# Kernel tuning notes

Measured on AMD Instinct MI355X. Metric: run time of the kernel, lower is better.

The kernel has to match this reference:

```python
import jax, jax.numpy as jnp
import numpy as np

N_NODES = 100000


def gcn_conv(x, edge_index, W, b):
    """PyG GCNConv: add self-loops, symmetric deg^{-1/2} A deg^{-1/2} aggregation.

    x: [N, Fin], edge_index: [2, E] int (row 0 = src, row 1 = dst).
    Transform first (Fin -> Fout), then gather-normalize-scatter at Fout.
    """
    n = x.shape[0]
    loops = jnp.arange(n, dtype=edge_index.dtype)
    src = jnp.concatenate([edge_index[0], loops])
    dst = jnp.concatenate([edge_index[1], loops])
    # in-degree with self-loops (all edge weights = 1)
    deg = jax.ops.segment_sum(jnp.ones_like(dst, dtype=x.dtype), dst, num_segments=n)
    dinv = jax.lax.rsqrt(deg)  # deg >= 1 thanks to self-loops
    norm = dinv[src] * dinv[dst]  # [E+N]
    h = x @ W  # [N, Fout] dense transform before sparse aggregation
    msgs = norm[:, None] * h[src]  # gather + normalize
    out = jax.ops.segment_sum(msgs, dst, num_segments=n)  # scatter-add
    return out + b


def setup_inputs() -> dict:
    key = jax.random.key(0)
    ks = jax.random.split(key, 8)
    N, E, Fin, H, C = N_NODES, 1600000, 256, 64, 11
    x = jax.random.normal(ks[0], (N, Fin), dtype=jnp.float32)
    edge_index = jax.random.randint(ks[1], (2, E), 0, N, dtype=jnp.int64)
    s1 = 1.0 / np.sqrt(Fin)
    s2 = 1.0 / np.sqrt(H)
    W1 = jax.random.uniform(ks[2], (Fin, H), jnp.float32, -s1, s1)
    b1 = jnp.zeros((H,), jnp.float32)
    W2 = jax.random.uniform(ks[3], (H, H), jnp.float32, -s2, s2)
    b2 = jnp.zeros((H,), jnp.float32)
    Wfc = jax.random.uniform(ks[4], (H, C), jnp.float32, -s2, s2)
    bfc = jax.random.uniform(ks[5], (C,), jnp.float32, -s2, s2)
    return {"x": x, "edge_index": edge_index, "W1": W1, "b1": b1,
            "W2": W2, "b2": b2, "Wfc": Wfc, "bfc": bfc}


def reference(x, edge_index, W1, b1, W2, b2, Wfc, bfc):
    h = jax.nn.relu(gcn_conv(x, edge_index, W1, b1))
    h = jax.nn.relu(gcn_conv(h, edge_index, W2, b2))
    return h @ Wfc + bfc  # [N, 11]
```

## Files before the change

kernel.cpp:

```cpp
#include <hip/hip_runtime.h>
#include <hip/hip_fp16.h>

#define NFEAT 64
#define CE 8192
#define EBUF 4608

typedef _Float16 half8 __attribute__((ext_vector_type(8)));
typedef float f32x4 __attribute__((ext_vector_type(4)));

__device__ __forceinline__ void gll16(const float* g, float* l) {
    __builtin_amdgcn_global_load_lds(
        (const __attribute__((address_space(1))) unsigned int*)g,
        (__attribute__((address_space(3))) unsigned int*)l, 16, 0, 0);
}

__device__ __forceinline__ __half2 bch(unsigned int u) {
    return __builtin_bit_cast(__half2, u);
}

__global__ void k_cvtW(const float* __restrict__ W, __half* __restrict__ Wt, int K) {
    int idx = blockIdx.x * 256 + threadIdx.x;
    if (idx >= 64 * K) return;
    int n = idx / K;
    int k = idx % K;
    Wt[idx] = __float2half(W[(size_t)k * NFEAT + n]);
}

template<int K, bool SCALE, bool CNT>
__global__ __launch_bounds__(256) void k_gemm_x(
    const float* __restrict__ A, const __half* __restrict__ Wt,
    const float* __restrict__ dinv, __half* __restrict__ H, int M,
    const int* __restrict__ eiDst, int* __restrict__ hist, int E)
{
    const int BM = 64, BK = 32;
    __shared__ float As[2 * BM * BK];

    int tid = threadIdx.x;
    int gemmIdx;
    if (CNT) {
        int bid = blockIdx.x;
        int nbkt = (M + 255) >> 8;
        if (bid % 9 == 8) {
            int c = bid / 9;
            int base = c * CE;
            if (base >= E) return;
            int* hb = (int*)As;
            for (int i = tid; i < nbkt; i += 256) hb[i] = 0;
            __syncthreads();
            int hi = min(base + CE, E);
            for (int e = base + tid; e < hi; e += 256)
                atomicAdd(&hb[eiDst[e] >> 8], 1);
            __syncthreads();
            for (int i = tid; i < nbkt; i += 256)
                hist[(size_t)c * nbkt + i] = hb[i];
            return;
        }
        gemmIdx = bid - bid / 9;
    } else {
        gemmIdx = blockIdx.x;
    }
    if (gemmIdx * BM >= M) return;

    int w = tid >> 6, lane = tid & 63;
    int q = lane >> 4, n16 = lane & 15;
    int m0 = gemmIdx * BM;

    auto stage = [&](int k0, int buf) {
#pragma unroll
        for (int rep = 0; rep < 2; ++rep) {
            int cb = (w * 2 + rep) * 64;
            int s = cb + lane;
            int m = s >> 3;
            int kk = (s & 7) ^ (m & 7);
            int row = m0 + m; if (row > M - 1) row = M - 1;
            gll16(A + (size_t)row * K + k0 + kk * 4,
                  &As[buf * (BM * BK) + cb * 4]);
        }
    };

    stage(0, 0);

    f32x4 acc[4];
#pragma unroll
    for (int nt = 0; nt < 4; ++nt) acc[nt] = (f32x4)(0.f);

    const __half* wp = Wt + (size_t)n16 * K + q * 8;

    const int T = K / BK;
    for (int kt = 0; kt < T; ++kt) {
        __syncthreads();
        if (kt + 1 < T) stage((kt + 1) * BK, (kt + 1) & 1);
        const float* As_ = &As[(kt & 1) * (BM * BK)];

        int ml = w * 16 + n16;
        int e0 = (2 * q) ^ (ml & 7);
        int e1 = (2 * q + 1) ^ (ml & 7);
        float4 f0 = *(const float4*)&As_[(ml * 8 + e0) * 4];
        float4 f1 = *(const float4*)&As_[(ml * 8 + e1) * 4];
        float fv[8] = {f0.x, f0.y, f0.z, f0.w, f1.x, f1.y, f1.z, f1.w};
        half8 ahi, alo;
#pragma unroll
        for (int j = 0; j < 8; ++j) {
            _Float16 hi = (_Float16)fv[j];
            ahi[j] = hi;
            alo[j] = (_Float16)(fv[j] - (float)hi);
        }
#pragma unroll
        for (int nt = 0; nt < 4; ++nt) {
            uint4 u = *(const uint4*)(wp + (size_t)(nt * 16) * K + kt * BK);
            half8 b = __builtin_bit_cast(half8, u);
            acc[nt] = __builtin_amdgcn_mfma_f32_16x16x32_f16(ahi, b, acc[nt], 0, 0, 0);
            acc[nt] = __builtin_amdgcn_mfma_f32_16x16x32_f16(alo, b, acc[nt], 0, 0, 0);
        }
        __syncthreads();
    }

#pragma unroll
    for (int reg = 0; reg < 4; ++reg) {
        int row = m0 + w * 16 + q * 4 + reg;
        if (row < M) {
            float di = SCALE ? dinv[row] : 1.0f;
#pragma unroll
            for (int nt = 0; nt < 4; ++nt)
                H[(size_t)row * NFEAT + nt * 16 + n16] =
                    __float2half(di * acc[nt][reg]);
        }
    }
}

__global__ __launch_bounds__(256) void k_scanB(int* __restrict__ hist,
                                               int* __restrict__ cntB,
                                               int nchk, int nbkt) {
    __shared__ int hb[256];
    int b = blockIdx.x, tid = threadIdx.x;
    int v = (tid < nchk) ? hist[(size_t)tid * nbkt + b] : 0;
    hb[tid] = v;
    __syncthreads();
    for (int off = 1; off < 256; off <<= 1) {
        int t = (tid >= off) ? hb[tid - off] : 0;
        __syncthreads();
        if (tid >= off) hb[tid] += t;
        __syncthreads();
    }
    if (tid < nchk) hist[(size_t)tid * nbkt + b] = hb[tid] - v;
    if (tid == 255) cntB[b] = hb[255];
}

__global__ __launch_bounds__(256) void k_scanC(const int* __restrict__ cntB,
                                               int* __restrict__ bb, int nbkt) {
    __shared__ int hb[256];
    int tid = threadIdx.x;
    int i0 = 2 * tid, i1 = 2 * tid + 1;
    int a0 = (i0 < nbkt) ? cntB[i0] : 0;
    int a1 = (i1 < nbkt) ? cntB[i1] : 0;
    hb[tid] = a0 + a1;
    __syncthreads();
    for (int off = 1; off < 256; off <<= 1) {
        int t = (tid >= off) ? hb[tid - off] : 0;
        __syncthreads();
        if (tid >= off) hb[tid] += t;
        __syncthreads();
    }
    int excl = hb[tid] - (a0 + a1);
    if (i0 <= nbkt) bb[i0] = excl;
    if (i1 <= nbkt) bb[i1] = excl + a0;
}

__global__ __launch_bounds__(256) void k_scatter(
    const int* __restrict__ ei, const int* __restrict__ hist,
    const int* __restrict__ bb, int2* __restrict__ E2, int E, int nbkt)
{
    __shared__ int ptr[512];
    int c = blockIdx.x, tid = threadIdx.x;
    for (int i = tid; i < nbkt; i += 256)
        ptr[i] = bb[i] + hist[(size_t)c * nbkt + i];
    __syncthreads();
    int base = c * CE, hi = min(base + CE, E);
    for (int e = base + tid; e < hi; e += 256) {
        int s = ei[e];
        int d = ei[(size_t)E + e];
        int p = atomicAdd(&ptr[d >> 8], 1);
        E2[p] = make_int2(s, d);
    }
}

__global__ __launch_bounds__(256) void k_csr(
    const int2* __restrict__ E2, const int* __restrict__ bb,
    int* __restrict__ rowptr, float* __restrict__ dinv, int* __restrict__ col,
    __half* __restrict__ A, int N, int E)
{
    __shared__ int2 ebuf[EBUF];
    __shared__ int cnt[256];
    __shared__ float dl[256];
    int b = blockIdx.x, tid = threadIdx.x;
    int e0 = bb[b], e1 = bb[b + 1], ne = e1 - e0;
    int nL = min(ne, EBUF);

    cnt[tid] = 0;
    __syncthreads();
    for (int i = tid; i < nL; i += 256) {
        int2 e = E2[e0 + i];
        ebuf[i] = e;
        atomicAdd(&cnt[e.y & 255], 1);
    }
    for (int i = nL + tid; i < ne; i += 256) {
        int2 e = E2[e0 + i];
        atomicAdd(&cnt[e.y & 255], 1);
    }
    __syncthreads();
    int c = cnt[tid];
    dl[tid] = rsqrtf((float)(c + 1));
    for (int off = 1; off < 256; off <<= 1) {
        int t = (tid >= off) ? cnt[tid - off] : 0;
        __syncthreads();
        if (tid >= off) cnt[tid] += t;
        __syncthreads();
    }
    int excl = cnt[tid] - c;
    int node = b * 256 + tid;
    if (node < N) {
        rowptr[node] = e0 + excl;
        dinv[node] = dl[tid];
    }
    if (b == 0 && tid == 0) rowptr[N] = E;
    __syncthreads();
    cnt[tid] = excl;
    __syncthreads();
    for (int i = tid; i < nL; i += 256) {
        int2 e = ebuf[i];
        int p = atomicAdd(&cnt[e.y & 255], 1);
        col[e0 + p] = e.x;
    }
    for (int i = nL + tid; i < ne; i += 256) {
        int2 e = E2[e0 + i];
        int p = atomicAdd(&cnt[e.y & 255], 1);
        col[e0 + p] = e.x;
    }

    for (int it = tid; it < 256 * 8; it += 256) {
        int ln = it >> 3;
        int node2 = b * 256 + ln;
        if (node2 < N) {
            float di = dl[ln];
            uint4* p = (uint4*)A + (size_t)node2 * 8 + (it & 7);
            uint4 u = *p;
            auto sc = [&](unsigned int x) {
                float2 f = __half22float2(bch(x));
                return __builtin_bit_cast(unsigned int,
                       __float22half2_rn(make_float2(f.x * di, f.y * di)));
            };
            u.x = sc(u.x); u.y = sc(u.y); u.z = sc(u.z); u.w = sc(u.w);
            *p = u;
        }
    }
}

template<bool FC>
__global__ __launch_bounds__(256) void k_aggr(
    const __half* __restrict__ h, const int* __restrict__ rowptr,
    const int* __restrict__ col, const float* __restrict__ dinv,
    const float* __restrict__ bias, const float* __restrict__ Wfc,
    const float* __restrict__ bfc, float* __restrict__ out, int n)
{
    __shared__ float Wl[NFEAT * 11 + 11];
    int tid = threadIdx.x;
    if (FC) {
        for (int i = tid; i < NFEAT * 11; i += 256) Wl[i] = Wfc[i];
        if (tid < 11) Wl[NFEAT * 11 + tid] = bfc[tid];
        __syncthreads();
    }
    int lane = tid & 63;
    int li = lane & 7;
    int fi = li << 3;
    int r = blockIdx.x * 32 + ((tid >> 6) << 3) + (lane >> 3);
    bool valid = r < n;

    int beg = 0, end = 0;
    if (valid) { beg = rowptr[r]; end = rowptr[r + 1]; }

    const __half* hp = h + fi;
    auto ld = [&](int src) { return *(const uint4*)(hp + (size_t)src * NFEAT); };

    float a0 = 0.f, a1 = 0.f, a2 = 0.f, a3 = 0.f,
          a4 = 0.f, a5 = 0.f, a6 = 0.f, a7 = 0.f;
    auto addu = [&](uint4 u) {
        float2 f0 = __half22float2(bch(u.x));
        float2 f1 = __half22float2(bch(u.y));
        float2 f2 = __half22float2(bch(u.z));
        float2 f3 = __half22float2(bch(u.w));
        a0 += f0.x; a1 += f0.y; a2 += f1.x; a3 += f1.y;
        a4 += f2.x; a5 += f2.y; a6 += f3.x; a7 += f3.y;
    };

    if (valid) addu(ld(r));
    int j = beg;
    for (; j + 1 < end; j += 2) {
        uint4 u0 = ld(col[j]);
        uint4 u1 = ld(col[j + 1]);
        uint4 s;
        s.x = __builtin_bit_cast(unsigned int, __hadd2(bch(u0.x), bch(u1.x)));
        s.y = __builtin_bit_cast(unsigned int, __hadd2(bch(u0.y), bch(u1.y)));
        s.z = __builtin_bit_cast(unsigned int, __hadd2(bch(u0.z), bch(u1.z)));
        s.w = __builtin_bit_cast(unsigned int, __hadd2(bch(u0.w), bch(u1.w)));
        addu(s);
    }
    if (j < end) addu(ld(col[j]));

    if (!valid) return;
    float di = dinv[r];
    float t0 = fmaxf(bias[fi + 0] + di * a0, 0.f);
    float t1 = fmaxf(bias[fi + 1] + di * a1, 0.f);
    float t2 = fmaxf(bias[fi + 2] + di * a2, 0.f);
    float t3 = fmaxf(bias[fi + 3] + di * a3, 0.f);
    float t4 = fmaxf(bias[fi + 4] + di * a4, 0.f);
    float t5 = fmaxf(bias[fi + 5] + di * a5, 0.f);
    float t6 = fmaxf(bias[fi + 6] + di * a6, 0.f);
    float t7 = fmaxf(bias[fi + 7] + di * a7, 0.f);

    if (!FC) {
        float4 lo = make_float4(t0, t1, t2, t3);
        float4 hi = make_float4(t4, t5, t6, t7);
        float* op = out + (size_t)r * NFEAT + fi;
        *(float4*)op = lo;
        *(float4*)(op + 4) = hi;
    } else {
#pragma unroll
        for (int c = 0; c < 11; ++c) {
            const float* wc = &Wl[fi * 11 + c];
            float p = t0 * wc[0] + t1 * wc[11] + t2 * wc[22] + t3 * wc[33]
                    + t4 * wc[44] + t5 * wc[55] + t6 * wc[66] + t7 * wc[77];
            p += __shfl_xor(p, 1, 64);
            p += __shfl_xor(p, 2, 64);
            p += __shfl_xor(p, 4, 64);
            if (li == 0) out[(size_t)r * 11 + c] = p + Wl[NFEAT * 11 + c];
        }
    }
}

extern "C" void kernel_launch(void* const* d_in, const int* in_sizes, int n_in,
                              void* d_out, int out_size, void* d_ws, size_t ws_size,
                              hipStream_t stream) {
    const float* x   = (const float*)d_in[0];
    const int*   ei  = (const int*)d_in[1];
    const float* W1  = (const float*)d_in[2];
    const float* b1  = (const float*)d_in[3];
    const float* W2  = (const float*)d_in[4];
    const float* b2  = (const float*)d_in[5];
    const float* Wfc = (const float*)d_in[6];
    const float* bfc = (const float*)d_in[7];
    float* out = (float*)d_out;

    const int Fin = 256;
    int N = in_sizes[0] / Fin;
    int E = in_sizes[1] / 2;

    char* ws = (char*)d_ws;
    size_t off = 0;
    auto alloc = [&](size_t bytes) { void* p = ws + off; off = (off + bytes + 255) & ~(size_t)255; return p; };
    int*    rowptr = (int*)   alloc((size_t)(N + 1) * 4);
    float*  dinv   = (float*) alloc((size_t)N * 4);
    int*    col    = (int*)   alloc((size_t)E * 4);
    __half* Wt1    = (__half*)alloc((size_t)64 * 256 * 2);
    __half* Wt2    = (__half*)alloc((size_t)64 * 64 * 2);
    __half* A      = (__half*)alloc((size_t)N * NFEAT * 2);
    float*  B      = (float*) alloc((size_t)N * NFEAT * 4);

    int NBKT = (N + 255) >> 8;
    int NCHK = (E + CE - 1) / CE;

    int2* E2   = (int2*)B;
    int*  hist = (int*)B + (size_t)2 * E;
    int*  bb   = hist + (size_t)NCHK * NBKT;
    int*  cntB = bb + NBKT + 1;

    int gE2 = NCHK;
    int gb  = (N + 63) / 64;
    int gA  = (N + 31) / 32;
    int g9  = 9 * max(NCHK, (gb + 7) / 8);

    k_cvtW<<<(64 * 256 + 255) / 256, 256, 0, stream>>>(W1, Wt1, 256);
    k_cvtW<<<(64 * 64 + 255) / 256, 256, 0, stream>>>(W2, Wt2, 64);

    k_gemm_x<256, false, true><<<g9, 256, 0, stream>>>(
        x, Wt1, nullptr, A, N, ei + E, hist, E);

    k_scanB<<<NBKT, 256, 0, stream>>>(hist, cntB, NCHK, NBKT);
    k_scanC<<<1, 256, 0, stream>>>(cntB, bb, NBKT);
    k_scatter<<<gE2, 256, 0, stream>>>(ei, hist, bb, E2, E, NBKT);
    k_csr<<<NBKT, 256, 0, stream>>>(E2, bb, rowptr, dinv, col, A, N, E);

    k_aggr<false><<<gA, 256, 0, stream>>>(A, rowptr, col, dinv, b1, nullptr, nullptr, B, N);

    k_gemm_x<64, true, false><<<gb, 256, 0, stream>>>(
        B, Wt2, dinv, A, N, nullptr, nullptr, 0);
    k_aggr<true><<<gA, 256, 0, stream>>>(A, rowptr, col, dinv, b2, Wfc, bfc, out, N);
}
```

Measured before the change: 327.1 us.

## Fuse layer-1 aggregation with layer-2 GEMM and restructure the preprocessing pipeline

Merges the two weight conversions and the edge histogram into a single prep kernel. The layer-1 GEMM now runs after CSR construction so it can apply the dinv scaling directly, which removes the separate rescale pass over A in k_csr. A new fused kernel aggregates layer 1 into shared memory and runs the 64x64 layer-2 GEMM with split-fp16 MFMA, so the fp32 intermediate no longer makes a global round-trip. The aggregation loops are unrolled to four gathers per iteration. In exchange, the big GEMM no longer overlaps with the histogram, and the fused kernel uses more LDS per block.

```diff
diff --git a/kernel.cpp b/kernel.cpp
--- a/kernel.cpp
+++ b/kernel.cpp
@@ -18,47 +18,46 @@
     return __builtin_bit_cast(__half2, u);
 }
 
-__global__ void k_cvtW(const float* __restrict__ W, __half* __restrict__ Wt, int K) {
-    int idx = blockIdx.x * 256 + threadIdx.x;
-    if (idx >= 64 * K) return;
-    int n = idx / K;
-    int k = idx % K;
-    Wt[idx] = __float2half(W[(size_t)k * NFEAT + n]);
-}
-
-template<int K, bool SCALE, bool CNT>
+__global__ __launch_bounds__(256) void k_prep(
+    const float* __restrict__ W1, __half* __restrict__ Wt1,
+    const float* __restrict__ W2, __half* __restrict__ Wt2,
+    const int* __restrict__ eiDst, int* __restrict__ hist, int E, int nbkt)
+{
+    __shared__ int hb[512];
+    int bid = blockIdx.x, tid = threadIdx.x;
+    if (bid < 64) {
+        int idx = bid * 256 + tid;
+        int n = idx >> 8, k = idx & 255;
+        Wt1[idx] = __float2half(W1[(size_t)k * NFEAT + n]);
+    } else if (bid < 80) {
+        int idx = (bid - 64) * 256 + tid;
+        int n = idx >> 6, k = idx & 63;
+        Wt2[idx] = __float2half(W2[(size_t)k * NFEAT + n]);
+    } else {
+        int c = bid - 80;
+        int base = c * CE;
+        if (base >= E) return;
+        for (int i = tid; i < nbkt; i += 256) hb[i] = 0;
+        __syncthreads();
+        int hi = min(base + CE, E);
+        for (int e = base + tid; e < hi; e += 256)
+            atomicAdd(&hb[eiDst[e] >> 8], 1);
+        __syncthreads();
+        for (int i = tid; i < nbkt; i += 256)
+            hist[(size_t)c * nbkt + i] = hb[i];
+    }
+}
+
+template<int K, bool SCALE>
 __global__ __launch_bounds__(256) void k_gemm_x(
     const float* __restrict__ A, const __half* __restrict__ Wt,
-    const float* __restrict__ dinv, __half* __restrict__ H, int M,
-    const int* __restrict__ eiDst, int* __restrict__ hist, int E)
+    const float* __restrict__ dinv, __half* __restrict__ H, int M)
 {
     const int BM = 64, BK = 32;
     __shared__ float As[2 * BM * BK];
 
     int tid = threadIdx.x;
-    int gemmIdx;
-    if (CNT) {
-        int bid = blockIdx.x;
-        int nbkt = (M + 255) >> 8;
-        if (bid % 9 == 8) {
-            int c = bid / 9;
-            int base = c * CE;
-            if (base >= E) return;
-            int* hb = (int*)As;
-            for (int i = tid; i < nbkt; i += 256) hb[i] = 0;
-            __syncthreads();
-            int hi = min(base + CE, E);
-            for (int e = base + tid; e < hi; e += 256)
-                atomicAdd(&hb[eiDst[e] >> 8], 1);
-            __syncthreads();
-            for (int i = tid; i < nbkt; i += 256)
-                hist[(size_t)c * nbkt + i] = hb[i];
-            return;
-        }
-        gemmIdx = bid - bid / 9;
-    } else {
-        gemmIdx = blockIdx.x;
-    }
+    int gemmIdx = blockIdx.x;
     if (gemmIdx * BM >= M) return;
 
     int w = tid >> 6, lane = tid & 63;
@@ -187,7 +186,7 @@
 __global__ __launch_bounds__(256) void k_csr(
     const int2* __restrict__ E2, const int* __restrict__ bb,
     int* __restrict__ rowptr, float* __restrict__ dinv, int* __restrict__ col,
-    __half* __restrict__ A, int N, int E)
+    int N, int E)
 {
     __shared__ int2 ebuf[EBUF];
     __shared__ int cnt[256];
@@ -236,27 +235,116 @@
         int p = atomicAdd(&cnt[e.y & 255], 1);
         col[e0 + p] = e.x;
     }
-
-    for (int it = tid; it < 256 * 8; it += 256) {
-        int ln = it >> 3;
-        int node2 = b * 256 + ln;
-        if (node2 < N) {
-            float di = dl[ln];
-            uint4* p = (uint4*)A + (size_t)node2 * 8 + (it & 7);
-            uint4 u = *p;
-            auto sc = [&](unsigned int x) {
-                float2 f = __half22float2(bch(x));
-                return __builtin_bit_cast(unsigned int,
-                       __float22half2_rn(make_float2(f.x * di, f.y * di)));
+}
+
+__global__ __launch_bounds__(256) void k_ag1g2(
+    const __half* __restrict__ h, const int* __restrict__ rowptr,
+    const int* __restrict__ col, const float* __restrict__ dinv,
+    const float* __restrict__ b1, const __half* __restrict__ Wt2,
+    __half* __restrict__ H2, int n)
+{
+    __shared__ float Bs[64][68];
+    int tid = threadIdx.x;
+    int w = tid >> 6, lane = tid & 63;
+    int li = lane & 7, fi = li << 3;
+    int slot = (w << 3) | (lane >> 3);
+
+    const __half* hp = h + fi;
+    auto ld = [&](int src) { return *(const uint4*)(hp + (size_t)src * NFEAT); };
+
+#pragma unroll
+    for (int hf = 0; hf < 2; ++hf) {
+        int lr = hf * 32 + slot;
+        int r = blockIdx.x * 64 + lr;
+        float t0 = 0.f, t1 = 0.f, t2 = 0.f, t3 = 0.f,
+              t4 = 0.f, t5 = 0.f, t6 = 0.f, t7 = 0.f;
+        if (r < n) {
+            float a0 = 0.f, a1 = 0.f, a2 = 0.f, a3 = 0.f,
+                  a4 = 0.f, a5 = 0.f, a6 = 0.f, a7 = 0.f;
+            auto addu = [&](uint4 u) {
+                float2 f0 = __half22float2(bch(u.x));
+                float2 f1 = __half22float2(bch(u.y));
+                float2 f2 = __half22float2(bch(u.z));
+                float2 f3 = __half22float2(bch(u.w));
+                a0 += f0.x; a1 += f0.y; a2 += f1.x; a3 += f1.y;
+                a4 += f2.x; a5 += f2.y; a6 += f3.x; a7 += f3.y;
             };
-            u.x = sc(u.x); u.y = sc(u.y); u.z = sc(u.z); u.w = sc(u.w);
-            *p = u;
-        }
-    }
-}
-
-template<bool FC>
-__global__ __launch_bounds__(256) void k_aggr(
+            auto p2 = [&](uint4 u0, uint4 u1) {
+                uint4 s;
+                s.x = __builtin_bit_cast(unsigned int, __hadd2(bch(u0.x), bch(u1.x)));
+                s.y = __builtin_bit_cast(unsigned int, __hadd2(bch(u0.y), bch(u1.y)));
+                s.z = __builtin_bit_cast(unsigned int, __hadd2(bch(u0.z), bch(u1.z)));
+                s.w = __builtin_bit_cast(unsigned int, __hadd2(bch(u0.w), bch(u1.w)));
+                addu(s);
+            };
+            int beg = rowptr[r], end = rowptr[r + 1];
+            addu(ld(r));
+            int j = beg;
+            for (; j + 3 < end; j += 4) {
+                uint4 u0 = ld(col[j]);
+                uint4 u1 = ld(col[j + 1]);
+                uint4 u2 = ld(col[j + 2]);
+                uint4 u3 = ld(col[j + 3]);
+                p2(u0, u1);
+                p2(u2, u3);
+            }
+            for (; j < end; ++j) addu(ld(col[j]));
+            float di = dinv[r];
+            t0 = fmaxf(b1[fi + 0] + di * a0, 0.f);
+            t1 = fmaxf(b1[fi + 1] + di * a1, 0.f);
+            t2 = fmaxf(b1[fi + 2] + di * a2, 0.f);
+            t3 = fmaxf(b1[fi + 3] + di * a3, 0.f);
+            t4 = fmaxf(b1[fi + 4] + di * a4, 0.f);
+            t5 = fmaxf(b1[fi + 5] + di * a5, 0.f);
+            t6 = fmaxf(b1[fi + 6] + di * a6, 0.f);
+            t7 = fmaxf(b1[fi + 7] + di * a7, 0.f);
+        }
+        *(float4*)&Bs[lr][fi]     = make_float4(t0, t1, t2, t3);
+        *(float4*)&Bs[lr][fi + 4] = make_float4(t4, t5, t6, t7);
+    }
+    __syncthreads();
+
+    int q = lane >> 4, n16 = lane & 15;
+    f32x4 acc[4];
+#pragma unroll
+    for (int nt = 0; nt < 4; ++nt) acc[nt] = (f32x4)(0.f);
+    const __half* wp = Wt2 + (size_t)n16 * 64 + q * 8;
+
+#pragma unroll
+    for (int kt = 0; kt < 2; ++kt) {
+        const float* ap = &Bs[w * 16 + n16][kt * 32 + q * 8];
+        float4 f0 = *(const float4*)ap;
+        float4 f1 = *(const float4*)(ap + 4);
+        float fv[8] = {f0.x, f0.y, f0.z, f0.w, f1.x, f1.y, f1.z, f1.w};
+        half8 ahi, alo;
+#pragma unroll
+        for (int j = 0; j < 8; ++j) {
+            _Float16 hi = (_Float16)fv[j];
+            ahi[j] = hi;
+            alo[j] = (_Float16)(fv[j] - (float)hi);
+        }
+#pragma unroll
+        for (int nt = 0; nt < 4; ++nt) {
+            uint4 u = *(const uint4*)(wp + (size_t)(nt * 16) * 64 + kt * 32);
+            half8 b = __builtin_bit_cast(half8, u);
+            acc[nt] = __builtin_amdgcn_mfma_f32_16x16x32_f16(ahi, b, acc[nt], 0, 0, 0);
+            acc[nt] = __builtin_amdgcn_mfma_f32_16x16x32_f16(alo, b, acc[nt], 0, 0, 0);
+        }
+    }
+#pragma unroll
+    for (int reg = 0; reg < 4; ++reg) {
+        int row = blockIdx.x * 64 + w * 16 + q * 4 + reg;
+        if (row < n) {
+            float di = dinv[row];
+#pragma unroll
+            for (int nt = 0; nt < 4; ++nt)
+                H2[(size_t)row * NFEAT + nt * 16 + n16] =
+                    __float2half(di * acc[nt][reg]);
+        }
+    }
+}
+
+__global__ __launch_bounds__(256) void k_aggr2(
     const __half* __restrict__ h, const int* __restrict__ rowptr,
     const int* __restrict__ col, const float* __restrict__ dinv,
     const float* __restrict__ bias, const float* __restrict__ Wfc,
@@ -264,11 +352,10 @@
 {
     __shared__ float Wl[NFEAT * 11 + 11];
     int tid = threadIdx.x;
-    if (FC) {
-        for (int i = tid; i < NFEAT * 11; i += 256) Wl[i] = Wfc[i];
-        if (tid < 11) Wl[NFEAT * 11 + tid] = bfc[tid];
-        __syncthreads();
-    }
+    for (int i = tid; i < NFEAT * 11; i += 256) Wl[i] = Wfc[i];
+    if (tid < 11) Wl[NFEAT * 11 + tid] = bfc[tid];
+    __syncthreads();
+
     int lane = tid & 63;
     int li = lane & 7;
     int fi = li << 3;
@@ -291,20 +378,26 @@
         a0 += f0.x; a1 += f0.y; a2 += f1.x; a3 += f1.y;
         a4 += f2.x; a5 += f2.y; a6 += f3.x; a7 += f3.y;
     };
-
-    if (valid) addu(ld(r));
-    int j = beg;
-    for (; j + 1 < end; j += 2) {
-        uint4 u0 = ld(col[j]);
-        uint4 u1 = ld(col[j + 1]);
+    auto p2 = [&](uint4 u0, uint4 u1) {
         uint4 s;
         s.x = __builtin_bit_cast(unsigned int, __hadd2(bch(u0.x), bch(u1.x)));
         s.y = __builtin_bit_cast(unsigned int, __hadd2(bch(u0.y), bch(u1.y)));
         s.z = __builtin_bit_cast(unsigned int, __hadd2(bch(u0.z), bch(u1.z)));
         s.w = __builtin_bit_cast(unsigned int, __hadd2(bch(u0.w), bch(u1.w)));
         addu(s);
-    }
-    if (j < end) addu(ld(col[j]));
+    };
+
+    if (valid) addu(ld(r));
+    int j = beg;
+    for (; j + 3 < end; j += 4) {
+        uint4 u0 = ld(col[j]);
+        uint4 u1 = ld(col[j + 1]);
+        uint4 u2 = ld(col[j + 2]);
+        uint4 u3 = ld(col[j + 3]);
+        p2(u0, u1);
+        p2(u2, u3);
+    }
+    for (; j < end; ++j) addu(ld(col[j]));
 
     if (!valid) return;
     float di = dinv[r];
@@ -317,23 +410,15 @@
     float t6 = fmaxf(bias[fi + 6] + di * a6, 0.f);
     float t7 = fmaxf(bias[fi + 7] + di * a7, 0.f);
 
-    if (!FC) {
-        float4 lo = make_float4(t0, t1, t2, t3);
-        float4 hi = make_float4(t4, t5, t6, t7);
-        float* op = out + (size_t)r * NFEAT + fi;
-        *(float4*)op = lo;
-        *(float4*)(op + 4) = hi;
-    } else {
-#pragma unroll
-        for (int c = 0; c < 11; ++c) {
-            const float* wc = &Wl[fi * 11 + c];
-            float p = t0 * wc[0] + t1 * wc[11] + t2 * wc[22] + t3 * wc[33]
-                    + t4 * wc[44] + t5 * wc[55] + t6 * wc[66] + t7 * wc[77];
-            p += __shfl_xor(p, 1, 64);
-            p += __shfl_xor(p, 2, 64);
-            p += __shfl_xor(p, 4, 64);
-            if (li == 0) out[(size_t)r * 11 + c] = p + Wl[NFEAT * 11 + c];
-        }
+#pragma unroll
+    for (int c = 0; c < 11; ++c) {
+        const float* wc = &Wl[fi * 11 + c];
+        float p = t0 * wc[0] + t1 * wc[11] + t2 * wc[22] + t3 * wc[33]
+                + t4 * wc[44] + t5 * wc[55] + t6 * wc[66] + t7 * wc[77];
+        p += __shfl_xor(p, 1, 64);
+        p += __shfl_xor(p, 2, 64);
+        p += __shfl_xor(p, 4, 64);
+        if (li == 0) out[(size_t)r * 11 + c] = p + Wl[NFEAT * 11 + c];
     }
 }
 
@@ -363,35 +448,29 @@
     __half* Wt1    = (__half*)alloc((size_t)64 * 256 * 2);
     __half* Wt2    = (__half*)alloc((size_t)64 * 64 * 2);
     __half* A      = (__half*)alloc((size_t)N * NFEAT * 2);
-    float*  B      = (float*) alloc((size_t)N * NFEAT * 4);
+    __half* H2     = (__half*)alloc((size_t)N * NFEAT * 2);
 
     int NBKT = (N + 255) >> 8;
     int NCHK = (E + CE - 1) / CE;
 
-    int2* E2   = (int2*)B;
-    int*  hist = (int*)B + (size_t)2 * E;
-    int*  bb   = hist + (size_t)NCHK * NBKT;
-    int*  cntB = bb + NBKT + 1;
-
-    int gE2 = NCHK;
-    int gb  = (N + 63) / 64;
-    int gA  = (N + 31) / 32;
-    int g9  = 9 * max(NCHK, (gb + 7) / 8);
-
-    k_cvtW<<<(64 * 256 + 255) / 256, 256, 0, stream>>>(W1, Wt1, 256);
-    k_cvtW<<<(64 * 64 + 255) / 256, 256, 0, stream>>>(W2, Wt2, 64);
-
-    k_gemm_x<256, false, true><<<g9, 256, 0, stream>>>(
-        x, Wt1, nullptr, A, N, ei + E, hist, E);
+    int2* E2   = (int2*)alloc((size_t)E * 8);
+    int*  hist = (int*) alloc((size_t)NCHK * NBKT * 4);
+    int*  bb   = (int*) alloc((size_t)(NBKT + 1) * 4);
+    int*  cntB = (int*) alloc((size_t)NBKT * 4);
+
+    int gb = (N + 63) / 64;
+    int gA = (N + 31) / 32;
+
+    k_prep<<<80 + NCHK, 256, 0, stream>>>(W1, Wt1, W2, Wt2, ei + E, hist, E, NBKT);
 
     k_scanB<<<NBKT, 256, 0, stream>>>(hist, cntB, NCHK, NBKT);
     k_scanC<<<1, 256, 0, stream>>>(cntB, bb, NBKT);
-    k_scatter<<<gE2, 256, 0, stream>>>(ei, hist, bb, E2, E, NBKT);
-    k_csr<<<NBKT, 256, 0, stream>>>(E2, bb, rowptr, dinv, col, A, N, E);
-
-    k_aggr<false><<<gA, 256, 0, stream>>>(A, rowptr, col, dinv, b1, nullptr, nullptr, B, N);
-
-    k_gemm_x<64, true, false><<<gb, 256, 0, stream>>>(
-        B, Wt2, dinv, A, N, nullptr, nullptr, 0);
-    k_aggr<true><<<gA, 256, 0, stream>>>(A, rowptr, col, dinv, b2, Wfc, bfc, out, N);
-}
+    k_scatter<<<NCHK, 256, 0, stream>>>(ei, hist, bb, E2, E, NBKT);
+    k_csr<<<NBKT, 256, 0, stream>>>(E2, bb, rowptr, dinv, col, N, E);
+
+    k_gemm_x<256, true><<<gb, 256, 0, stream>>>(x, Wt1, dinv, A, N);
+
+    k_ag1g2<<<gb, 256, 0, stream>>>(A, rowptr, col, dinv, b1, Wt2, H2, N);
+
+    k_aggr2<<<gA, 256, 0, stream>>>(H2, rowptr, col, dinv, b2, Wfc, bfc, out, N);
+}
```

Result: no change. 327.3 us (+0.1%).
